# Kernel tuning notes

Hardware: AMD Instinct MI355X
Metric: run time of the kernel (lower is better)

The kernel has to match this reference:

```python
import jax, jax.numpy as jnp
import numpy as np

B, C_IN, H, W = 8, 64, 64, 64
C_MID = 32


def setup_inputs() -> dict:
    key = jax.random.key(0)
    ks = jax.random.split(key, 7)
    s = 1.0 / np.sqrt(C_IN)
    return {
        "x": jax.random.normal(ks[0], (B, C_IN, H, W), dtype=jnp.float32),
        "Wk": jax.random.normal(ks[1], (C_MID, C_IN), dtype=jnp.float32) * s,
        "bk": jax.random.normal(ks[2], (C_MID,), dtype=jnp.float32) * 0.01,
        "Wq": jax.random.normal(ks[3], (C_MID, C_IN), dtype=jnp.float32) * s,
        "bq": jax.random.normal(ks[4], (C_MID,), dtype=jnp.float32) * 0.01,
        "Wv": jax.random.normal(ks[5], (C_MID, C_IN), dtype=jnp.float32) * s,
        "bv": jax.random.normal(ks[6], (C_MID,), dtype=jnp.float32) * 0.01,
    }


def reference(x, Wk, bk, Wq, bq, Wv, bv):
    # 1x1 convs == per-pixel channel projections
    def proj(Wt, bt):
        return jnp.einsum('bchw,oc->bohw', x, Wt) + bt[None, :, None, None]

    k = proj(Wk, bk)  # [B, Cm, H, W]
    q = proj(Wq, bq)
    v = proj(Wv, bv)

    b, c, h, w = q.shape
    n = h * w
    qf = q.reshape(b, c, n)
    kf = k.reshape(b, c, n)
    vf = v.reshape(b, c, n)

    # correlated_weight over spatial dims [2,3]: QK channel correlation per
    # pixel pair, softmax over key positions, weighted sum of V.
    scores = jnp.einsum('bcn,bcm->bnm', qf, kf)      # [B, N, N]
    attn = jax.nn.softmax(scores, axis=-1)
    out = jnp.einsum('bnm,bcm->bcn', attn, vf)       # [B, Cm, N]
    return out.reshape(b, c, h, w)
```

## Files before the change

### kernel.cpp

```cpp
#include <hip/hip_runtime.h>
#include <hip/hip_bf16.h>
#include <cstdint>
#include <cstddef>


typedef _Float16 f16x8 __attribute__((ext_vector_type(8)));
typedef float  f32x16 __attribute__((ext_vector_type(16)));
typedef float  f32x4  __attribute__((ext_vector_type(4)));

struct alignas(16) U4 { uint32_t w[4]; };
struct alignas(8)  U2 { uint32_t w[2]; };

#define MFMA16(A, B, C) __builtin_amdgcn_mfma_f32_32x32x16_f16((A), (B), (C), 0, 0, 0)

__device__ __forceinline__ uint16_t f2h(float f) {
    _Float16 h = (_Float16)f;
    return __builtin_bit_cast(uint16_t, h);
}
__device__ __forceinline__ uint32_t cvtpk16(float lo, float hi) {
    auto h2 = __builtin_amdgcn_cvt_pkrtz(lo, hi);
    return __builtin_bit_cast(uint32_t, h2);
}
__device__ __forceinline__ void swp(uint32_t& a, uint32_t& b) {
    asm("v_permlane32_swap_b32 %0, %1" : "+v"(a), "+v"(b));
}
__device__ __forceinline__ float ex2(float x) {
    float r;
    asm("v_exp_f32 %0, %1" : "=v"(r) : "v"(x));
    return r;
}
__device__ __forceinline__ float max3(float a, float b, float c) {
    return fmaxf(fmaxf(a, b), c);
}
__device__ __forceinline__ f16x8 ld8(const void* p) {
    return __builtin_bit_cast(f16x8, *(const U4*)p);
}
__device__ __forceinline__ void gload16(const void* g, void* l) {
    __builtin_amdgcn_global_load_lds(
        (const __attribute__((address_space(1))) void*)g,
        (__attribute__((address_space(3))) void*)l, 16, 0, 0);
}

__global__ __launch_bounds__(256) void proj_kernel(
    const float* __restrict__ x,
    const float* __restrict__ Wk, const float* __restrict__ bk,
    const float* __restrict__ Wq, const float* __restrict__ bq,
    const float* __restrict__ Wv, const float* __restrict__ bv,
    uint16_t* __restrict__ qf, uint16_t* __restrict__ kf,
    uint16_t* __restrict__ vt)
{
    const int g     = blockIdx.x * 256 + threadIdx.x;
    const int pixel = g & 32767;
    const int qt    = __builtin_amdgcn_readfirstlane(g >> 15);
    const int b     = pixel >> 12;
    const int n     = pixel & 4095;
    const int ob    = qt << 2;

    const float* xb = x + (size_t)b * 64 * 4096 + n;
    float xv[64];
    #pragma unroll
    for (int ci = 0; ci < 64; ++ci) xv[ci] = xb[(size_t)ci * 4096];

    #pragma unroll
    for (int pass = 0; pass < 3; ++pass) {
        const float* W    = pass == 0 ? Wk : (pass == 1 ? Wq : Wv);
        const float* bias = pass == 0 ? bk : (pass == 1 ? bq : bv);
        float acc[4];
        #pragma unroll
        for (int o = 0; o < 4; ++o) acc[o] = bias[ob + o];
        #pragma unroll
        for (int o = 0; o < 4; ++o) {
            const float* wr = W + (size_t)(ob + o) * 64;
            #pragma unroll
            for (int ci = 0; ci < 64; ++ci)
                acc[o] = fmaf(wr[ci], xv[ci], acc[o]);
        }
        if (pass == 2) {
            #pragma unroll
            for (int o = 0; o < 4; ++o) {
                int c   = ob + o;
                int nsw = (n & ~0x38) | ((((n >> 3) & 7) ^ (c & 7)) << 3);
                vt[((size_t)(b * 32 + c)) * 4096 + nsw] = f2h(acc[o]);
            }
        } else {
            if (pass == 1) {
                #pragma unroll
                for (int o = 0; o < 4; ++o) acc[o] *= 1.44269504f;
            }
            U2 hp;
            #pragma unroll
            for (int j = 0; j < 2; ++j)
                hp.w[j] = (uint32_t)f2h(acc[2 * j]) | ((uint32_t)f2h(acc[2 * j + 1]) << 16);
            if (pass == 0) {
                char* rowb = (char*)kf + ((size_t)(b * 4096 + n)) * 64;
                *(U2*)(rowb + (((qt >> 1) ^ (n & 3)) * 16) + (qt & 1) * 8) = hp;
            } else {
                uint16_t* hd = qf + ((size_t)(b * 4096 + n)) * 32 + ob;
                *(U2*)hd = hp;
            }
        }
    }
}

__global__ __launch_bounds__(256, 4) void attn_kernel(
    const uint16_t* __restrict__ qf, const uint16_t* __restrict__ kf,
    const uint16_t* __restrict__ vt, float* __restrict__ out,
    float* __restrict__ opart, float* __restrict__ mpart,
    float* __restrict__ lpart, int ns)
{
    __shared__ __align__(16) char lds_k[2][4096];
    __shared__ __align__(16) char lds_v[2][4096];

    const int blk    = blockIdx.x;
    const int b      = blk & 7;
    const int rest   = blk >> 3;
    const int qblk   = rest & 31;
    const int ksp    = rest >> 5;
    const int ntiles = 64 / ns;
    const int kb0    = ksp * ntiles;
    const int kb1    = kb0 + ntiles;

    const int tid  = threadIdx.x;
    const int wv   = __builtin_amdgcn_readfirstlane(tid >> 6);
    const int lane = tid & 63;
    const int l31  = lane & 31;
    const int h32  = lane >> 5;
    const int qrow = qblk * 128 + wv * 32 + l31;

    f16x8 q0, q1;
    {
        const uint16_t* r = qf + ((size_t)(b * 4096 + qrow)) * 32;
        q0 = ld8(r + h32 * 8);
        q1 = ld8(r + 16 + h32 * 8);
    }

    f32x16 oacc;
    #pragma unroll
    for (int i = 0; i < 16; ++i) oacc[i] = 0.f;
    float m_run = -3.0e38f, l_run = 0.f;

    const char* gk = (const char*)kf + ((size_t)b * 4096) * 64;
    const char* gv = (const char*)vt
                   + ((size_t)(b * 32 + wv * 8 + (lane >> 3))) * 8192
                   + (lane & 7) * 16;
    const char* gk_l = gk + wv * 1024 + lane * 16;

    const int ka0 = l31 * 64 + ((h32 ^ (l31 & 3)) * 16);
    const int ka1 = l31 * 64 + (((2 + h32) ^ (l31 & 3)) * 16);
    int vo[4];
    #pragma unroll
    for (int j = 0; j < 4; ++j)
        vo[j] = l31 * 128 + (((h32 + 2 * j) ^ (l31 & 7)) * 16);

    {
        gload16(gk_l + (size_t)kb0 * 4096, lds_k[kb0 & 1] + wv * 1024);
        gload16(gv   + (size_t)kb0 * 128,  lds_v[kb0 & 1] + wv * 1024);
    }

    #pragma unroll 2
    for (int kb = kb0; kb < kb1; ++kb) {
        const int cur = kb & 1;
        __syncthreads();

        if (kb + 1 < kb1) {
            gload16(gk_l + (size_t)(kb + 1) * 4096, lds_k[cur ^ 1] + wv * 1024);
            gload16(gv   + (size_t)(kb + 1) * 128,  lds_v[cur ^ 1] + wv * 1024);
        }

        f32x16 s0, s1;
        #pragma unroll
        for (int i = 0; i < 16; ++i) { s0[i] = 0.f; s1[i] = 0.f; }
        {
            const char* lk = lds_k[cur];
            f16x8 a0 = ld8(lk + ka0);
            f16x8 a1 = ld8(lk + ka1);
            f16x8 c0 = ld8(lk + 2048 + ka0);
            f16x8 c1 = ld8(lk + 2048 + ka1);
            s0 = MFMA16(a0, q0, s0);
            s1 = MFMA16(c0, q0, s1);
            s0 = MFMA16(a1, q1, s0);
            s1 = MFMA16(c1, q1, s1);
        }

        float mx[4];
        #pragma unroll
        for (int i = 0; i < 4; ++i)
            mx[i] = max3(max3(s0[i], s0[i + 4], s0[i + 8]),
                         max3(s0[i + 12], s1[i], s1[i + 4]),
                         fmaxf(s1[i + 8], s1[i + 12]));
        float pm = fmaxf(max3(mx[0], mx[1], mx[2]), mx[3]);
        pm = fmaxf(pm, __shfl_xor(pm, 32));

        if (__any(pm > m_run)) {
            float mn  = fmaxf(m_run, pm);
            float scl = ex2(m_run - mn);
            l_run *= scl;
            #pragma unroll
            for (int i = 0; i < 16; ++i) oacc[i] *= scl;
            m_run = mn;
        }

        #pragma unroll
        for (int i = 0; i < 16; ++i) {
            s0[i] = ex2(s0[i] - m_run);
            s1[i] = ex2(s1[i] - m_run);
        }
        float sm[8];
        #pragma unroll
        for (int i = 0; i < 8; ++i)
            sm[i] = (s0[i] + s0[i + 8]) + (s1[i] + s1[i + 8]);
        #pragma unroll
        for (int i = 0; i < 4; ++i) sm[i] += sm[i + 4];
        float rs = (sm[0] + sm[2]) + (sm[1] + sm[3]);
        rs += __shfl_xor(rs, 32);
        l_run += rs;

        U4 f1, f2, f3, f4;
        {
            uint32_t A = cvtpk16(s0[0], s0[1]),  B = cvtpk16(s0[4], s0[5]);   swp(A, B);
            uint32_t C = cvtpk16(s0[2], s0[3]),  D = cvtpk16(s0[6], s0[7]);   swp(C, D);
            f1.w[0] = A; f1.w[1] = C; f1.w[2] = B; f1.w[3] = D;
            A = cvtpk16(s0[8], s0[9]);   B = cvtpk16(s0[12], s0[13]);  swp(A, B);
            C = cvtpk16(s0[10], s0[11]); D = cvtpk16(s0[14], s0[15]);  swp(C, D);
            f2.w[0] = A; f2.w[1] = C; f2.w[2] = B; f2.w[3] = D;
            A = cvtpk16(s1[0], s1[1]);   B = cvtpk16(s1[4], s1[5]);    swp(A, B);
            C = cvtpk16(s1[2], s1[3]);   D = cvtpk16(s1[6], s1[7]);    swp(C, D);
            f3.w[0] = A; f3.w[1] = C; f3.w[2] = B; f3.w[3] = D;
            A = cvtpk16(s1[8], s1[9]);   B = cvtpk16(s1[12], s1[13]);  swp(A, B);
            C = cvtpk16(s1[10], s1[11]); D = cvtpk16(s1[14], s1[15]);  swp(C, D);
            f4.w[0] = A; f4.w[1] = C; f4.w[2] = B; f4.w[3] = D;
        }

        {
            const char* lv = lds_v[cur];
            f16x8 v0 = ld8(lv + vo[0]);
            f16x8 v1 = ld8(lv + vo[1]);
            f16x8 v2 = ld8(lv + vo[2]);
            f16x8 v3 = ld8(lv + vo[3]);
            oacc = MFMA16(v0, __builtin_bit_cast(f16x8, f1), oacc);
            oacc = MFMA16(v1, __builtin_bit_cast(f16x8, f2), oacc);
            oacc = MFMA16(v2, __builtin_bit_cast(f16x8, f3), oacc);
            oacc = MFMA16(v3, __builtin_bit_cast(f16x8, f4), oacc);
        }
    }

    if (ns == 1) {
        const float inv = 1.f / l_run;
        float* ob = out + ((size_t)b * 32) * 4096 + qrow;
        #pragma unroll
        for (int i = 0; i < 16; ++i) {
            int c = (i & 3) + 8 * (i >> 2) + 4 * h32;
            ob[(size_t)c * 4096] = oacc[i] * inv;
        }
    } else {
        float* op = opart + ((size_t)((ksp * 8 + b) * 32)) * 4096 + qrow;
        #pragma unroll
        for (int i = 0; i < 16; ++i) {
            int c = (i & 3) + 8 * (i >> 2) + 4 * h32;
            op[(size_t)c * 4096] = oacc[i];
        }
        if (h32 == 0) {
            mpart[((size_t)(ksp * 8 + b)) * 4096 + qrow] = m_run;
            lpart[((size_t)(ksp * 8 + b)) * 4096 + qrow] = l_run;
        }
    }
}

__global__ __launch_bounds__(256) void reduce_kernel(
    const float* __restrict__ opart, const float* __restrict__ mpart,
    const float* __restrict__ lpart, float* __restrict__ out, int ns)
{
    const int idx = blockIdx.x * 256 + threadIdx.x;
    const int nq  = idx & 1023;
    const int c   = (idx >> 10) & 31;
    const int b   = idx >> 15;
    const size_t noff = (size_t)nq * 4;

    f32x4 M;
    #pragma unroll
    for (int e = 0; e < 4; ++e) M[e] = -3.0e38f;
    for (int s = 0; s < ns; ++s) {
        f32x4 mm = *(const f32x4*)(mpart + ((size_t)(s * 8 + b)) * 4096 + noff);
        #pragma unroll
        for (int e = 0; e < 4; ++e) M[e] = fmaxf(M[e], mm[e]);
    }
    f32x4 L, O;
    #pragma unroll
    for (int e = 0; e < 4; ++e) { L[e] = 0.f; O[e] = 0.f; }
    for (int s = 0; s < ns; ++s) {
        f32x4 mm = *(const f32x4*)(mpart + ((size_t)(s * 8 + b)) * 4096 + noff);
        f32x4 ll = *(const f32x4*)(lpart + ((size_t)(s * 8 + b)) * 4096 + noff);
        f32x4 oo = *(const f32x4*)(opart + ((size_t)((s * 8 + b) * 32 + c)) * 4096 + noff);
        #pragma unroll
        for (int e = 0; e < 4; ++e) {
            float w = ex2(mm[e] - M[e]);
            L[e] += ll[e] * w;
            O[e] += oo[e] * w;
        }
    }
    f32x4 r;
    #pragma unroll
    for (int e = 0; e < 4; ++e) r[e] = O[e] / L[e];
    *(f32x4*)(out + ((size_t)(b * 32 + c)) * 4096 + noff) = r;
}

extern "C" void kernel_launch(void* const* d_in, const int* in_sizes, int n_in,
                              void* d_out, int out_size, void* d_ws, size_t ws_size,
                              hipStream_t stream)
{
    (void)in_sizes; (void)n_in; (void)out_size;
    const float* x  = (const float*)d_in[0];
    const float* Wk = (const float*)d_in[1];
    const float* bk = (const float*)d_in[2];
    const float* Wq = (const float*)d_in[3];
    const float* bq = (const float*)d_in[4];
    const float* Wv = (const float*)d_in[5];
    const float* bv = (const float*)d_in[6];
    float* out = (float*)d_out;

    char* ws = (char*)d_ws;
    const size_t SZ = (size_t)8 * 4096 * 32 * 2;
    uint16_t* qf = (uint16_t*)(ws);
    uint16_t* kf = (uint16_t*)(ws + SZ);
    uint16_t* vt = (uint16_t*)(ws + 2 * SZ);
    const size_t base = 3 * SZ;

    const size_t OB  = (size_t)8 * 32 * 4096 * 4;
    const size_t MB_ = (size_t)8 * 4096 * 4;
    int ns = 1;
    if      (ws_size >= base + 4 * (OB + 2 * MB_)) ns = 4;
    else if (ws_size >= base + 2 * (OB + 2 * MB_)) ns = 2;

    float* opart = (float*)(ws + base);
    float* mpart = (float*)(ws + base + (size_t)ns * OB);
    float* lpart = (float*)(ws + base + (size_t)ns * OB + (size_t)ns * MB_);

    proj_kernel<<<1024, 256, 0, stream>>>(x, Wk, bk, Wq, bq, Wv, bv,
                                          qf, kf, vt);
    attn_kernel<<<ns * 256, 256, 0, stream>>>(qf, kf, vt, out,
                                              opart, mpart, lpart, ns);
    if (ns > 1)
        reduce_kernel<<<1024, 256, 0, stream>>>(opart, mpart, lpart, out, ns);
}
```

Before: 63.86 us.

## Process two key tiles per barrier and defer softmax max rescaling

The attention loop now loads and processes two K/V tiles per iteration with doubled LDS buffers, halving the number of __syncthreads barriers and prefetch issues per key block. The running max is only rescaled when a new tile max exceeds the old by more than 6 (log2 units), which skips most oacc rescales. Score accumulators start from a shared zero vector instead of being zeroed each tile. LDS per block doubles to 32KB, which could limit occupancy, and the lazy max threshold allows exponentials up to 2^6 in fp16 P values, with some precision risk.

```diff
diff --git a/kernel.cpp b/kernel.cpp
--- a/kernel.cpp
+++ b/kernel.cpp
@@ -108,8 +108,8 @@
     float* __restrict__ opart, float* __restrict__ mpart,
     float* __restrict__ lpart, int ns)
 {
-    __shared__ __align__(16) char lds_k[2][4096];
-    __shared__ __align__(16) char lds_v[2][4096];
+    __shared__ __align__(16) char lds_k[2][2][4096];
+    __shared__ __align__(16) char lds_v[2][2][4096];
 
     const int blk    = blockIdx.x;
     const int b      = blk & 7;
@@ -118,7 +118,7 @@
     const int ksp    = rest >> 5;
     const int ntiles = 64 / ns;
     const int kb0    = ksp * ntiles;
-    const int kb1    = kb0 + ntiles;
+    const int niter  = ntiles >> 1;
 
     const int tid  = threadIdx.x;
     const int wv   = __builtin_amdgcn_readfirstlane(tid >> 6);
@@ -134,15 +134,15 @@
         q1 = ld8(r + 16 + h32 * 8);
     }
 
-    f32x16 oacc;
-    #pragma unroll
-    for (int i = 0; i < 16; ++i) oacc[i] = 0.f;
+    f32x16 oacc, zf;
+    #pragma unroll
+    for (int i = 0; i < 16; ++i) { oacc[i] = 0.f; zf[i] = 0.f; }
     float m_run = -3.0e38f, l_run = 0.f;
 
-    const char* gk = (const char*)kf + ((size_t)b * 4096) * 64;
-    const char* gv = (const char*)vt
-                   + ((size_t)(b * 32 + wv * 8 + (lane >> 3))) * 8192
-                   + (lane & 7) * 16;
+    const char* gk   = (const char*)kf + ((size_t)b * 4096) * 64;
+    const char* gv   = (const char*)vt
+                     + ((size_t)(b * 32 + wv * 8 + (lane >> 3))) * 8192
+                     + (lane & 7) * 16;
     const char* gk_l = gk + wv * 1024 + lane * 16;
 
     const int ka0 = l31 * 64 + ((h32 ^ (l31 & 3)) * 16);
@@ -152,96 +152,102 @@
     for (int j = 0; j < 4; ++j)
         vo[j] = l31 * 128 + (((h32 + 2 * j) ^ (l31 & 7)) * 16);
 
-    {
-        gload16(gk_l + (size_t)kb0 * 4096, lds_k[kb0 & 1] + wv * 1024);
-        gload16(gv   + (size_t)kb0 * 128,  lds_v[kb0 & 1] + wv * 1024);
-    }
-
-    #pragma unroll 2
-    for (int kb = kb0; kb < kb1; ++kb) {
-        const int cur = kb & 1;
+    gload16(gk_l + (size_t)kb0 * 4096,       lds_k[0][0] + wv * 1024);
+    gload16(gv   + (size_t)kb0 * 128,        lds_v[0][0] + wv * 1024);
+    gload16(gk_l + (size_t)(kb0 + 1) * 4096, lds_k[0][1] + wv * 1024);
+    gload16(gv   + (size_t)(kb0 + 1) * 128,  lds_v[0][1] + wv * 1024);
+
+    int p = 0;
+    #pragma unroll 1
+    for (int it = 0; it < niter; ++it) {
         __syncthreads();
 
-        if (kb + 1 < kb1) {
-            gload16(gk_l + (size_t)(kb + 1) * 4096, lds_k[cur ^ 1] + wv * 1024);
-            gload16(gv   + (size_t)(kb + 1) * 128,  lds_v[cur ^ 1] + wv * 1024);
-        }
-
-        f32x16 s0, s1;
-        #pragma unroll
-        for (int i = 0; i < 16; ++i) { s0[i] = 0.f; s1[i] = 0.f; }
-        {
-            const char* lk = lds_k[cur];
-            f16x8 a0 = ld8(lk + ka0);
-            f16x8 a1 = ld8(lk + ka1);
-            f16x8 c0 = ld8(lk + 2048 + ka0);
-            f16x8 c1 = ld8(lk + 2048 + ka1);
-            s0 = MFMA16(a0, q0, s0);
-            s1 = MFMA16(c0, q0, s1);
-            s0 = MFMA16(a1, q1, s0);
-            s1 = MFMA16(c1, q1, s1);
-        }
-
-        float mx[4];
-        #pragma unroll
-        for (int i = 0; i < 4; ++i)
-            mx[i] = max3(max3(s0[i], s0[i + 4], s0[i + 8]),
-                         max3(s0[i + 12], s1[i], s1[i + 4]),
-                         fmaxf(s1[i + 8], s1[i + 12]));
-        float pm = fmaxf(max3(mx[0], mx[1], mx[2]), mx[3]);
-        pm = fmaxf(pm, __shfl_xor(pm, 32));
-
-        if (__any(pm > m_run)) {
-            float mn  = fmaxf(m_run, pm);
-            float scl = ex2(m_run - mn);
-            l_run *= scl;
-            #pragma unroll
-            for (int i = 0; i < 16; ++i) oacc[i] *= scl;
-            m_run = mn;
-        }
-
-        #pragma unroll
-        for (int i = 0; i < 16; ++i) {
-            s0[i] = ex2(s0[i] - m_run);
-            s1[i] = ex2(s1[i] - m_run);
-        }
-        float sm[8];
-        #pragma unroll
-        for (int i = 0; i < 8; ++i)
-            sm[i] = (s0[i] + s0[i + 8]) + (s1[i] + s1[i + 8]);
-        #pragma unroll
-        for (int i = 0; i < 4; ++i) sm[i] += sm[i + 4];
-        float rs = (sm[0] + sm[2]) + (sm[1] + sm[3]);
-        rs += __shfl_xor(rs, 32);
-        l_run += rs;
-
-        U4 f1, f2, f3, f4;
-        {
-            uint32_t A = cvtpk16(s0[0], s0[1]),  B = cvtpk16(s0[4], s0[5]);   swp(A, B);
-            uint32_t C = cvtpk16(s0[2], s0[3]),  D = cvtpk16(s0[6], s0[7]);   swp(C, D);
-            f1.w[0] = A; f1.w[1] = C; f1.w[2] = B; f1.w[3] = D;
-            A = cvtpk16(s0[8], s0[9]);   B = cvtpk16(s0[12], s0[13]);  swp(A, B);
-            C = cvtpk16(s0[10], s0[11]); D = cvtpk16(s0[14], s0[15]);  swp(C, D);
-            f2.w[0] = A; f2.w[1] = C; f2.w[2] = B; f2.w[3] = D;
-            A = cvtpk16(s1[0], s1[1]);   B = cvtpk16(s1[4], s1[5]);    swp(A, B);
-            C = cvtpk16(s1[2], s1[3]);   D = cvtpk16(s1[6], s1[7]);    swp(C, D);
-            f3.w[0] = A; f3.w[1] = C; f3.w[2] = B; f3.w[3] = D;
-            A = cvtpk16(s1[8], s1[9]);   B = cvtpk16(s1[12], s1[13]);  swp(A, B);
-            C = cvtpk16(s1[10], s1[11]); D = cvtpk16(s1[14], s1[15]);  swp(C, D);
-            f4.w[0] = A; f4.w[1] = C; f4.w[2] = B; f4.w[3] = D;
-        }
-
-        {
-            const char* lv = lds_v[cur];
-            f16x8 v0 = ld8(lv + vo[0]);
-            f16x8 v1 = ld8(lv + vo[1]);
-            f16x8 v2 = ld8(lv + vo[2]);
-            f16x8 v3 = ld8(lv + vo[3]);
-            oacc = MFMA16(v0, __builtin_bit_cast(f16x8, f1), oacc);
-            oacc = MFMA16(v1, __builtin_bit_cast(f16x8, f2), oacc);
-            oacc = MFMA16(v2, __builtin_bit_cast(f16x8, f3), oacc);
-            oacc = MFMA16(v3, __builtin_bit_cast(f16x8, f4), oacc);
-        }
+        if (it + 1 < niter) {
+            const int tn = kb0 + 2 * it + 2;
+            gload16(gk_l + (size_t)tn * 4096,       lds_k[p ^ 1][0] + wv * 1024);
+            gload16(gv   + (size_t)tn * 128,        lds_v[p ^ 1][0] + wv * 1024);
+            gload16(gk_l + (size_t)(tn + 1) * 4096, lds_k[p ^ 1][1] + wv * 1024);
+            gload16(gv   + (size_t)(tn + 1) * 128,  lds_v[p ^ 1][1] + wv * 1024);
+        }
+
+        #pragma unroll
+        for (int sl = 0; sl < 2; ++sl) {
+            const char* lk = lds_k[p][sl];
+            const char* lv = lds_v[p][sl];
+
+            f32x16 s0, s1;
+            {
+                f16x8 a0 = ld8(lk + ka0);
+                f16x8 a1 = ld8(lk + ka1);
+                f16x8 c0 = ld8(lk + 2048 + ka0);
+                f16x8 c1 = ld8(lk + 2048 + ka1);
+                s0 = MFMA16(a0, q0, zf);
+                s1 = MFMA16(c0, q0, zf);
+                s0 = MFMA16(a1, q1, s0);
+                s1 = MFMA16(c1, q1, s1);
+            }
+
+            float mx[4];
+            #pragma unroll
+            for (int i = 0; i < 4; ++i)
+                mx[i] = max3(max3(s0[i], s0[i + 4], s0[i + 8]),
+                             max3(s0[i + 12], s1[i], s1[i + 4]),
+                             fmaxf(s1[i + 8], s1[i + 12]));
+            float pm = fmaxf(max3(mx[0], mx[1], mx[2]), mx[3]);
+            pm = fmaxf(pm, __shfl_xor(pm, 32));
+
+            if (__any(pm > m_run + 6.f)) {
+                float mn  = fmaxf(m_run, pm);
+                float scl = ex2(m_run - mn);
+                l_run *= scl;
+                #pragma unroll
+                for (int i = 0; i < 16; ++i) oacc[i] *= scl;
+                m_run = mn;
+            }
+
+            #pragma unroll
+            for (int i = 0; i < 16; ++i) {
+                s0[i] = ex2(s0[i] - m_run);
+                s1[i] = ex2(s1[i] - m_run);
+            }
+            float sm[8];
+            #pragma unroll
+            for (int i = 0; i < 8; ++i)
+                sm[i] = (s0[i] + s0[i + 8]) + (s1[i] + s1[i + 8]);
+            #pragma unroll
+            for (int i = 0; i < 4; ++i) sm[i] += sm[i + 4];
+            float rs = (sm[0] + sm[2]) + (sm[1] + sm[3]);
+            rs += __shfl_xor(rs, 32);
+            l_run += rs;
+
+            U4 f1, f2, f3, f4;
+            {
+                uint32_t A = cvtpk16(s0[0], s0[1]),  B = cvtpk16(s0[4], s0[5]);   swp(A, B);
+                uint32_t C = cvtpk16(s0[2], s0[3]),  D = cvtpk16(s0[6], s0[7]);   swp(C, D);
+                f1.w[0] = A; f1.w[1] = C; f1.w[2] = B; f1.w[3] = D;
+                A = cvtpk16(s0[8], s0[9]);   B = cvtpk16(s0[12], s0[13]);  swp(A, B);
+                C = cvtpk16(s0[10], s0[11]); D = cvtpk16(s0[14], s0[15]);  swp(C, D);
+                f2.w[0] = A; f2.w[1] = C; f2.w[2] = B; f2.w[3] = D;
+                A = cvtpk16(s1[0], s1[1]);   B = cvtpk16(s1[4], s1[5]);    swp(A, B);
+                C = cvtpk16(s1[2], s1[3]);   D = cvtpk16(s1[6], s1[7]);    swp(C, D);
+                f3.w[0] = A; f3.w[1] = C; f3.w[2] = B; f3.w[3] = D;
+                A = cvtpk16(s1[8], s1[9]);   B = cvtpk16(s1[12], s1[13]);  swp(A, B);
+                C = cvtpk16(s1[10], s1[11]); D = cvtpk16(s1[14], s1[15]);  swp(C, D);
+                f4.w[0] = A; f4.w[1] = C; f4.w[2] = B; f4.w[3] = D;
+            }
+
+            {
+                f16x8 v0 = ld8(lv + vo[0]);
+                f16x8 v1 = ld8(lv + vo[1]);
+                f16x8 v2 = ld8(lv + vo[2]);
+                f16x8 v3 = ld8(lv + vo[3]);
+                oacc = MFMA16(v0, __builtin_bit_cast(f16x8, f1), oacc);
+                oacc = MFMA16(v1, __builtin_bit_cast(f16x8, f2), oacc);
+                oacc = MFMA16(v2, __builtin_bit_cast(f16x8, f3), oacc);
+                oacc = MFMA16(v3, __builtin_bit_cast(f16x8, f4), oacc);
+            }
+        }
+        p ^= 1;
     }
 
     if (ns == 1) {
```

Measured after the change: 62.31 us. 2.4% less time.
